# Kernel tuning notes

Measured on AMD Instinct MI355X. Metric: run time of the kernel, lower is better.

The kernel has to match this reference:

```python
import math
import jax, jax.numpy as jnp
import numpy as np

NUM_HEADS = 16
EPS = 1e-6


def _rotate_half(t):
    t1, t2 = jnp.split(t, 2, axis=-1)
    return jnp.concatenate([-t2, t1], axis=-1)


def _rmsnorm(t, w):
    # compute in fp32 like the torch module, then cast back and apply affine
    x32 = t.astype(jnp.float32)
    r = jax.lax.rsqrt(jnp.mean(x32 * x32, axis=-1, keepdims=True) + EPS)
    return (x32 * r).astype(t.dtype) * w


def setup_inputs() -> dict:
    key = jax.random.key(0)
    ks = jax.random.split(key, 12)
    B, N, C, T = 8, 1024, 1024, 1024
    hd2 = (C // NUM_HEADS) // 2  # 32
    inp = {
        "x": jax.random.normal(ks[0], (B, N, C), jnp.float32),
        "temb": jax.random.normal(ks[1], (B, T), jnp.float32),
        "cos_y": jax.random.uniform(ks[2], (1, 1, N, hd2), jnp.float32, -1.0, 1.0),
        "sin_y": jax.random.uniform(ks[3], (1, 1, N, hd2), jnp.float32, -1.0, 1.0),
        "cos_x": jax.random.uniform(ks[4], (1, 1, N, hd2), jnp.float32, -1.0, 1.0),
        "sin_x": jax.random.uniform(ks[5], (1, 1, N, hd2), jnp.float32, -1.0, 1.0),
        # params; weights stored (in, out) so y = x @ W + b (== torch x @ W.T)
        "Wqkv": jax.random.normal(ks[6], (C, 3 * C), jnp.float32) * 0.02,
        "bqkv": jnp.zeros((3 * C,), jnp.float32),
        "Wt": jax.random.normal(ks[7], (T, 3 * C), jnp.float32) * 0.02,
        "bt": jnp.zeros((3 * C,), jnp.float32),
        "Wp": jax.random.normal(ks[8], (C, C), jnp.float32) * 0.02,
        "bp": jnp.zeros((C,), jnp.float32),
        "qn_w": jnp.ones((C // NUM_HEADS,), jnp.float32),
        "kn_w": jnp.ones((C // NUM_HEADS,), jnp.float32),
    }
    return inp


def reference(x, temb, cos_y, sin_y, cos_x, sin_x,
              Wqkv, bqkv, Wt, bt, Wp, bp, qn_w, kn_w):
    B, N, C = x.shape
    H = NUM_HEADS
    hd = C // H
    # fused QKV projection + additive time conditioning
    qkv = x @ Wqkv + bqkv + (temb @ Wt + bt)[:, None, :]         # [B,N,3C]
    qkv = qkv.reshape(B, N, 3, H, hd).transpose(2, 0, 3, 1, 4)    # [3,B,H,N,hd]
    q, k, v = qkv[0], qkv[1], qkv[2]
    # per-head QK RMSNorm with affine
    q = _rmsnorm(q, qn_w)
    k = _rmsnorm(k, kn_w)
    # axial 2D RoPE on the y-half and x-half of head_dim
    qy, qx = jnp.split(q, 2, axis=-1)
    ky, kx = jnp.split(k, 2, axis=-1)
    qy = qy * cos_y + _rotate_half(qy) * sin_y
    ky = ky * cos_y + _rotate_half(ky) * sin_y
    qx = qx * cos_x + _rotate_half(qx) * sin_x
    kx = kx * cos_x + _rotate_half(kx) * sin_x
    q = jnp.concatenate([qy, qx], axis=-1)
    k = jnp.concatenate([ky, kx], axis=-1)
    # scaled dot-product attention (no dropout at eval)
    scale = 1.0 / math.sqrt(hd)
    scores = jnp.einsum('bhqd,bhkd->bhqk', q, k) * scale
    attn = jax.nn.softmax(scores, axis=-1)
    out = jnp.einsum('bhqk,bhkd->bhqd', attn, v)                  # [B,H,N,hd]
    out = out.transpose(0, 2, 1, 3).reshape(B, N, C)
    return out @ Wp + bp
```

## Files before the change

### kernel.cpp

```cpp
#include <hip/hip_runtime.h>
#include <cstdint>

typedef unsigned short u16;
typedef __bf16 bf16x8 __attribute__((ext_vector_type(8)));
typedef float f32x4 __attribute__((ext_vector_type(4)));

__device__ __forceinline__ u16 f2bf(float f) {
  __bf16 h = (__bf16)f;
  return __builtin_bit_cast(u16, h);
}
__device__ __forceinline__ float bf2f(u16 u) {
  union { uint32_t u; float f; } v; v.u = ((uint32_t)u) << 16;
  return v.f;
}

__device__ __forceinline__ void gload16(const void* g, const void* l) {
  __builtin_amdgcn_global_load_lds(
      (const __attribute__((address_space(1))) uint32_t*)(uintptr_t)g,
      (__attribute__((address_space(3))) uint32_t*)(uintptr_t)l, 16, 0, 0);
}

__device__ __forceinline__ f32x4 mfma16(bf16x8 a, bf16x8 b, f32x4 c) {
  return __builtin_amdgcn_mfma_f32_16x16x32_bf16(a, b, c, 0, 0, 0);
}

__device__ __forceinline__ int swz(int row, int col) {
  return row * 64 + ((((col >> 3) ^ (row & 7)) << 3) | (col & 7));
}

__device__ __forceinline__ void transpose64(const float* __restrict__ src,
                                            u16* __restrict__ dst, int R, int Cc,
                                            int r0, int c0, u16* t) {
  #pragma unroll
  for (int i = 0; i < 16; i++) {
    int e = i * 256 + threadIdx.x;
    int rl = e >> 6, cl = e & 63;
    t[cl * 66 + rl] = f2bf(src[(size_t)(r0 + rl) * Cc + c0 + cl]);
  }
  __syncthreads();
  #pragma unroll
  for (int i = 0; i < 16; i++) {
    int e = i * 256 + threadIdx.x;
    int ro = e >> 6, co = e & 63;
    dst[(size_t)(c0 + ro) * R + r0 + co] = t[ro * 66 + co];
  }
}

__global__ __launch_bounds__(256)
void k_prep(const float* __restrict__ x, u16* __restrict__ x_bf,
            const float* __restrict__ Wqkv, u16* __restrict__ WqkvT,
            const float* __restrict__ Wp, u16* __restrict__ WpT,
            const float* __restrict__ temb, const float* __restrict__ Wt,
            float* __restrict__ tpart) {
  __shared__ u16 t[64 * 66];
  int bid = blockIdx.x;
  if (bid < 8192) {
    int i = bid * 256 + threadIdx.x;
    float4 v = ((const float4*)x)[i];
    union { u16 s[4]; uint2 u; } o;
    o.s[0] = f2bf(v.x); o.s[1] = f2bf(v.y); o.s[2] = f2bf(v.z); o.s[3] = f2bf(v.w);
    ((uint2*)x_bf)[i] = o.u;
    return;
  }
  bid -= 8192;
  if (bid < 768) {
    transpose64(Wqkv, WqkvT, 1024, 3072, (bid / 48) * 64, (bid % 48) * 64, t);
    return;
  }
  bid -= 768;
  if (bid < 256) {
    transpose64(Wp, WpT, 1024, 1024, (bid / 16) * 64, (bid % 16) * 64, t);
    return;
  }
  bid -= 256;
  {
    const int j = (bid % 12) * 256 + threadIdx.x;
    const int k0 = (bid / 12) * 32;
    float acc[8];
    #pragma unroll
    for (int b = 0; b < 8; b++) acc[b] = 0.f;
    #pragma unroll 4
    for (int k = k0; k < k0 + 32; k++) {
      float wv = Wt[(size_t)k * 3072 + j];
      #pragma unroll
      for (int b = 0; b < 8; b++) acc[b] += temb[b * 1024 + k] * wv;
    }
    float* p = tpart + (size_t)(bid / 12) * 24576 + j;
    #pragma unroll
    for (int b = 0; b < 8; b++) p[b * 3072] = acc[b];
  }
}

template <int MODE>
__global__ __launch_bounds__(512, 2)
void k_gemm(const u16* __restrict__ A, const u16* __restrict__ Bt,
            u16* __restrict__ outb, float* __restrict__ outf,
            const float* __restrict__ bias,
            const float* __restrict__ bt, const float* __restrict__ bqkv,
            const float* __restrict__ tpart, int K, int Ntot) {
  __shared__ __align__(16) u16 As[3][128 * 64];
  __shared__ __align__(16) u16 Bs[3][256 * 64];
  __shared__ float tcs[256];

  const int nb = (int)gridDim.x;
  const int bid = (int)blockIdx.x;
  const int sb = (bid & 7) * (nb >> 3) + (bid >> 3);
  const int NBN = Ntot >> 8;
  const int m0 = (sb / NBN) * 128;
  const int n0 = (sb % NBN) * 256;

  const int lane = threadIdx.x & 63;
  const int w = threadIdx.x >> 6;
  const int wm = w >> 2;
  const int wn = w & 3;
  const int l15 = lane & 15;
  const int g8 = (lane >> 4) * 8;
  const int lr = lane >> 3;
  const int schunk = ((lane & 7) ^ lr) * 8;

  const u16* Ag = A + (size_t)(m0 + w * 16 + lr) * K + schunk;
  const u16* Bg = Bt + (size_t)(n0 + lr) * K + schunk;

  if (MODE == 0) {
    if (threadIdx.x < 256) {
      const int bidx = m0 >> 10;
      const int j = n0 + (int)threadIdx.x;
      float a = bt[j] + bqkv[j];
      #pragma unroll
      for (int kt = 0; kt < 32; kt++) a += tpart[(size_t)kt * 24576 + bidx * 3072 + j];
      tcs[threadIdx.x] = a;
    }
    asm volatile("" ::: "memory");
  }

  f32x4 acc[4][4];
  #pragma unroll
  for (int i = 0; i < 4; i++)
    #pragma unroll
    for (int j = 0; j < 4; j++) acc[i][j] = (f32x4){0.f, 0.f, 0.f, 0.f};

  auto stageA_Blo = [&](int kt_, int buf_) {
    const int ko = kt_ << 6;
    #pragma unroll
    for (int t = 0; t < 2; t++) {
      int r0 = w * 16 + t * 8;
      gload16(Ag + (size_t)(t * 8) * K + ko, &As[buf_][r0 * 64]);
    }
    #pragma unroll
    for (int t = 0; t < 2; t++) {
      int f0 = w * 16 + t * 8;
      int r0 = (f0 >> 5) * 64 + (f0 & 31);
      gload16(Bg + (size_t)r0 * K + ko, &Bs[buf_][r0 * 64]);
    }
  };
  auto stageBhi = [&](int kt_, int buf_) {
    const int ko = kt_ << 6;
    #pragma unroll
    for (int t = 0; t < 2; t++) {
      int f0 = w * 16 + t * 8;
      int r0 = (f0 >> 5) * 64 + 32 + (f0 & 31);
      gload16(Bg + (size_t)r0 * K + ko, &Bs[buf_][r0 * 64]);
    }
  };

  const int NT = K >> 6;
  stageA_Blo(0, 0); stageBhi(0, 0);
  stageA_Blo(1, 1); stageBhi(1, 1);
  asm volatile("s_waitcnt vmcnt(8)" ::: "memory");
  __builtin_amdgcn_s_barrier();
  asm volatile("" ::: "memory");

  int cur = 0;
  for (int kt = 0; kt < NT; kt++) {
    const int nxtbuf = cur + 2 >= 3 ? cur - 1 : cur + 2;

    bf16x8 af[2][4], bfr[2][4];
    #pragma unroll
    for (int s = 0; s < 2; s++)
      #pragma unroll
      for (int mf = 0; mf < 4; mf++)
        af[s][mf] = *(const bf16x8*)&As[cur][swz(wm * 64 + mf * 16 + l15, s * 32 + g8)];
    #pragma unroll
    for (int s = 0; s < 2; s++)
      #pragma unroll
      for (int nf = 0; nf < 2; nf++)
        bfr[s][nf] = *(const bf16x8*)&Bs[cur][swz(wn * 64 + nf * 16 + l15, s * 32 + g8)];
    if (kt + 2 < NT) stageA_Blo(kt + 2, nxtbuf);
    if (kt <= NT - 2) asm volatile("s_waitcnt vmcnt(6)" ::: "memory");
    else              asm volatile("s_waitcnt vmcnt(0)" ::: "memory");
    __builtin_amdgcn_s_barrier();
    asm volatile("" ::: "memory");
    __builtin_amdgcn_s_setprio(1);
    #pragma unroll
    for (int s = 0; s < 2; s++)
      #pragma unroll
      for (int mf = 0; mf < 4; mf++)
        #pragma unroll
        for (int nf = 0; nf < 2; nf++)
          acc[mf][nf] = mfma16(af[s][mf], bfr[s][nf], acc[mf][nf]);
    __builtin_amdgcn_s_setprio(0);

    #pragma unroll
    for (int s = 0; s < 2; s++)
      #pragma unroll
      for (int nf = 2; nf < 4; nf++)
        bfr[s][nf] = *(const bf16x8*)&Bs[cur][swz(wn * 64 + nf * 16 + l15, s * 32 + g8)];
    if (kt + 2 < NT) stageBhi(kt + 2, nxtbuf);
    if (kt < NT - 2)       asm volatile("s_waitcnt vmcnt(6)" ::: "memory");
    else if (kt == NT - 2) asm volatile("s_waitcnt vmcnt(2)" ::: "memory");
    else                   asm volatile("s_waitcnt vmcnt(0)" ::: "memory");
    __builtin_amdgcn_s_barrier();
    asm volatile("" ::: "memory");
    __builtin_amdgcn_s_setprio(1);
    #pragma unroll
    for (int s = 0; s < 2; s++)
      #pragma unroll
      for (int mf = 0; mf < 4; mf++)
        #pragma unroll
        for (int nf = 2; nf < 4; nf++)
          acc[mf][nf] = mfma16(af[s][mf], bfr[s][nf], acc[mf][nf]);
    __builtin_amdgcn_s_setprio(0);

    cur = cur + 1 >= 3 ? 0 : cur + 1;
  }

  const int rl = (lane >> 4) * 4;
  #pragma unroll
  for (int mf = 0; mf < 4; mf++) {
    #pragma unroll
    for (int nf = 0; nf < 4; nf++) {
      #pragma unroll
      for (int r = 0; r < 4; r++) {
        int grow = m0 + wm * 64 + mf * 16 + rl + r;
        int gcol = n0 + wn * 64 + nf * 16 + l15;
        float v = acc[mf][nf][r];
        if (MODE == 0) {
          v += tcs[wn * 64 + nf * 16 + l15];
          outb[(size_t)grow * Ntot + gcol] = f2bf(v);
        } else {
          v += bias[gcol];
          outf[(size_t)grow * Ntot + gcol] = v;
        }
      }
    }
  }
}

__global__ __launch_bounds__(256)
void k_rrv(const u16* __restrict__ qkv,
           const float* __restrict__ cos_y, const float* __restrict__ sin_y,
           const float* __restrict__ cos_x, const float* __restrict__ sin_x,
           const float* __restrict__ qn_w, const float* __restrict__ kn_w,
           u16* __restrict__ Qo, u16* __restrict__ Ko, u16* __restrict__ VT) {
  __shared__ u16 t[64 * 68];
  const int n0 = blockIdx.x * 64, h = blockIdx.y, b = blockIdx.z;
  const int bh = b * 16 + h;
  const int lane = threadIdx.x & 63, w = threadIdx.x >> 6;
  const int l15 = lane & 15, lg = lane >> 4;
  float4 qw = *(const float4*)(qn_w + l15 * 4);
  float4 kw = *(const float4*)(kn_w + l15 * 4);
  const float sgn = (lane & 4) ? 1.0f : -1.0f;
  const float* ct = (lane & 8) ? cos_x : cos_y;
  const float* st = (lane & 8) ? sin_x : sin_y;
  const float QSCALE = 0.18033688011112042f;

  #pragma unroll
  for (int rr = 0; rr < 4; rr++) {
    int row = n0 + w * 16 + rr * 4 + lg;
    size_t src = (size_t)(b * 1024 + row) * 3072 + h * 64 + l15 * 4;
    uint2 qu = *(const uint2*)(qkv + src);
    uint2 ku = *(const uint2*)(qkv + src + 1024);
    float q[4], k[4];
    q[0] = bf2f((u16)qu.x); q[1] = bf2f((u16)(qu.x >> 16));
    q[2] = bf2f((u16)qu.y); q[3] = bf2f((u16)(qu.y >> 16));
    k[0] = bf2f((u16)ku.x); k[1] = bf2f((u16)(ku.x >> 16));
    k[2] = bf2f((u16)ku.y); k[3] = bf2f((u16)(ku.y >> 16));
    float sq = q[0]*q[0] + q[1]*q[1] + q[2]*q[2] + q[3]*q[3];
    float sk = k[0]*k[0] + k[1]*k[1] + k[2]*k[2] + k[3]*k[3];
    #pragma unroll
    for (int m = 1; m < 16; m <<= 1) {
      sq += __shfl_xor(sq, m);
      sk += __shfl_xor(sk, m);
    }
    float rq = rsqrtf(sq * (1.0f / 64.0f) + 1e-6f);
    float rk = rsqrtf(sk * (1.0f / 64.0f) + 1e-6f);
    float4 cc = *(const float4*)(ct + (size_t)row * 32 + (lane & 7) * 4);
    float4 ss = *(const float4*)(st + (size_t)row * 32 + (lane & 7) * 4);
    float qn[4], kn[4];
    qn[0] = q[0]*rq*qw.x; qn[1] = q[1]*rq*qw.y; qn[2] = q[2]*rq*qw.z; qn[3] = q[3]*rq*qw.w;
    kn[0] = k[0]*rk*kw.x; kn[1] = k[1]*rk*kw.y; kn[2] = k[2]*rk*kw.z; kn[3] = k[3]*rk*kw.w;
    float c[4] = {cc.x, cc.y, cc.z, cc.w};
    float s[4] = {ss.x, ss.y, ss.z, ss.w};
    union { u16 e[4]; uint2 u; } oq, ok;
    #pragma unroll
    for (int j = 0; j < 4; j++) {
      float qp = __shfl_xor(qn[j], 4);
      float kp = __shfl_xor(kn[j], 4);
      oq.e[j] = f2bf((qn[j] * c[j] + sgn * qp * s[j]) * QSCALE);
      ok.e[j] = f2bf(kn[j] * c[j] + sgn * kp * s[j]);
    }
    size_t dst = ((size_t)bh * 1024 + row) * 64 + l15 * 4;
    *(uint2*)(Qo + dst) = oq.u;
    *(uint2*)(Ko + dst) = ok.u;
  }

  #pragma unroll
  for (int i = 0; i < 4; i++) {
    int e = i * 256 + threadIdx.x;
    int n = e >> 4, dc = e & 15;
    uint2 v = *(const uint2*)(qkv + (size_t)(b * 1024 + n0 + n) * 3072 + 2048 + h * 64 + dc * 4);
    t[(dc * 4 + 0) * 68 + n] = (u16)v.x;
    t[(dc * 4 + 1) * 68 + n] = (u16)(v.x >> 16);
    t[(dc * 4 + 2) * 68 + n] = (u16)v.y;
    t[(dc * 4 + 3) * 68 + n] = (u16)(v.y >> 16);
  }
  __syncthreads();
  #pragma unroll
  for (int i = 0; i < 4; i++) {
    int e = i * 256 + threadIdx.x;
    int d = e >> 4, nc = e & 15;
    const u16* p = &t[d * 68 + nc * 4];
    uint2 o;
    o.x = (uint32_t)p[0] | ((uint32_t)p[1] << 16);
    o.y = (uint32_t)p[2] | ((uint32_t)p[3] << 16);
    *(uint2*)(VT + ((size_t)bh * 64 + d) * 1024 + n0 + nc * 4) = o;
  }
}

__global__ __launch_bounds__(256, 2)
void k_attn(const u16* __restrict__ Q, const u16* __restrict__ Kb,
            const u16* __restrict__ VT, u16* __restrict__ Ob) {
  __shared__ u16 Ks[2][4096], VTs[2][4096], Ps[4][2048];
  const int lane = threadIdx.x & 63;
  const int w = threadIdx.x >> 6;
  const int bh = blockIdx.x;
  const int qt = blockIdx.y;
  const int b = bh >> 4, h = bh & 15;
  const size_t base = (size_t)bh * 65536;
  const int q0 = qt * 128;
  const int scol = ((lane & 7) ^ (lane >> 3)) * 8;
  const int lr = lane >> 3;

  bf16x8 aq[2][2];
  #pragma unroll
  for (int i = 0; i < 2; i++)
    #pragma unroll
    for (int s = 0; s < 2; s++)
      aq[i][s] = *(const bf16x8*)(Q + base +
          (size_t)(q0 + w * 32 + i * 16 + (lane & 15)) * 64 + s * 32 + (lane >> 4) * 8);

  f32x4 acc_o[2][4];
  float lpar[2][4];
  #pragma unroll
  for (int i = 0; i < 2; i++)
    #pragma unroll
    for (int r = 0; r < 4; r++) {
      acc_o[i][r] = (f32x4){0.f, 0.f, 0.f, 0.f};
      lpar[i][r] = 0.f;
    }

  #pragma unroll
  for (int tt = 0; tt < 2; tt++) {
    int t = w * 2 + tt;
    gload16(Kb + base + (size_t)(8 * t + lr) * 64 + scol, &Ks[0][t * 512]);
    gload16(VT + base + (size_t)(8 * t + lr) * 1024 + scol, &VTs[0][t * 512]);
  }

  for (int it = 0; it < 16; it++) {
    __syncthreads();
    const int cur = it & 1;
    if (it < 15) {
      const int nxt = cur ^ 1;
      const int j1 = (it + 1) * 64;
      #pragma unroll
      for (int tt = 0; tt < 2; tt++) {
        int t = w * 2 + tt;
        gload16(Kb + base + (size_t)(j1 + 8 * t + lr) * 64 + scol, &Ks[nxt][t * 512]);
        gload16(VT + base + (size_t)(8 * t + lr) * 1024 + j1 + scol, &VTs[nxt][t * 512]);
      }
    }
    const u16* K_ = Ks[cur];
    const u16* V_ = VTs[cur];

    f32x4 accs[2][4];
    #pragma unroll
    for (int i = 0; i < 2; i++)
      #pragma unroll
      for (int nt = 0; nt < 4; nt++) accs[i][nt] = (f32x4){0.f, 0.f, 0.f, 0.f};
    #pragma unroll
    for (int s = 0; s < 2; s++) {
      bf16x8 bk[4];
      #pragma unroll
      for (int nt = 0; nt < 4; nt++)
        bk[nt] = *(const bf16x8*)&K_[swz(nt * 16 + (lane & 15), s * 32 + (lane >> 4) * 8)];
      __builtin_amdgcn_s_setprio(1);
      #pragma unroll
      for (int i = 0; i < 2; i++)
        #pragma unroll
        for (int nt = 0; nt < 4; nt++)
          accs[i][nt] = mfma16(aq[i][s], bk[nt], accs[i][nt]);
      __builtin_amdgcn_s_setprio(0);
    }

    #pragma unroll
    for (int i = 0; i < 2; i++) {
      #pragma unroll
      for (int nt = 0; nt < 4; nt++) {
        #pragma unroll
        for (int r = 0; r < 4; r++) {
          float p = __builtin_amdgcn_exp2f(accs[i][nt][r]);
          lpar[i][r] += p;
          Ps[w][swz(i * 16 + (lane >> 4) * 4 + r, nt * 16 + (lane & 15))] = f2bf(p);
        }
      }
    }
    asm volatile("s_waitcnt lgkmcnt(0)" ::: "memory");

    #pragma unroll
    for (int s = 0; s < 2; s++) {
      bf16x8 bv[4];
      #pragma unroll
      for (int dt = 0; dt < 4; dt++)
        bv[dt] = *(const bf16x8*)&V_[swz(dt * 16 + (lane & 15), s * 32 + (lane >> 4) * 8)];
      bf16x8 ap0 = *(const bf16x8*)&Ps[w][swz(0 * 16 + (lane & 15), s * 32 + (lane >> 4) * 8)];
      bf16x8 ap1 = *(const bf16x8*)&Ps[w][swz(1 * 16 + (lane & 15), s * 32 + (lane >> 4) * 8)];
      __builtin_amdgcn_s_setprio(1);
      #pragma unroll
      for (int dt = 0; dt < 4; dt++) {
        acc_o[0][dt] = mfma16(ap0, bv[dt], acc_o[0][dt]);
        acc_o[1][dt] = mfma16(ap1, bv[dt], acc_o[1][dt]);
      }
      __builtin_amdgcn_s_setprio(0);
    }
  }

  #pragma unroll
  for (int i = 0; i < 2; i++) {
    float inv[4];
    #pragma unroll
    for (int r = 0; r < 4; r++) {
      float l = lpar[i][r];
      #pragma unroll
      for (int m = 1; m < 16; m <<= 1) l += __shfl_xor(l, m);
      inv[r] = 1.0f / l;
    }
    #pragma unroll
    for (int dt = 0; dt < 4; dt++)
      #pragma unroll
      for (int r = 0; r < 4; r++) {
        int row = q0 + w * 32 + i * 16 + (lane >> 4) * 4 + r;
        int col = h * 64 + dt * 16 + (lane & 15);
        Ob[((size_t)b * 1024 + row) * 1024 + col] = f2bf(acc_o[i][dt][r] * inv[r]);
      }
  }
}

extern "C" void kernel_launch(void* const* d_in, const int* in_sizes, int n_in,
                              void* d_out, int out_size, void* d_ws, size_t ws_size,
                              hipStream_t stream) {
  const float* x     = (const float*)d_in[0];
  const float* temb  = (const float*)d_in[1];
  const float* cos_y = (const float*)d_in[2];
  const float* sin_y = (const float*)d_in[3];
  const float* cos_x = (const float*)d_in[4];
  const float* sin_x = (const float*)d_in[5];
  const float* Wqkv  = (const float*)d_in[6];
  const float* bqkv  = (const float*)d_in[7];
  const float* Wt    = (const float*)d_in[8];
  const float* bt    = (const float*)d_in[9];
  const float* Wp    = (const float*)d_in[10];
  const float* bp    = (const float*)d_in[11];
  const float* qn_w  = (const float*)d_in[12];
  const float* kn_w  = (const float*)d_in[13];
  float* out = (float*)d_out;

  char* ws = (char*)d_ws;
  u16*   x_bf  = (u16*)(ws);
  u16*   WqkvT = (u16*)(ws + 16777216);
  u16*   WpT   = (u16*)(ws + 23068672);
  u16*   qkv   = (u16*)(ws + 25264128);
  u16*   Qb    = (u16*)(ws + 75595776);
  u16*   Kb    = (u16*)(ws + 92372992);
  u16*   VTb   = (u16*)(ws + 109150208);
  float* tpart = (float*)(ws + 125927424);
  u16*   att   = x_bf;

  k_prep<<<9600, 256, 0, stream>>>(x, x_bf, Wqkv, WqkvT, Wp, WpT, temb, Wt, tpart);
  k_gemm<0><<<dim3(768), 512, 0, stream>>>(x_bf, WqkvT, qkv, nullptr, nullptr,
                                           bt, bqkv, tpart, 1024, 3072);
  k_rrv<<<dim3(16, 16, 8), 256, 0, stream>>>(qkv, cos_y, sin_y, cos_x, sin_x,
                                             qn_w, kn_w, Qb, Kb, VTb);
  k_attn<<<dim3(128, 8), 256, 0, stream>>>(Qb, Kb, VTb, att);
  k_gemm<1><<<dim3(256), 512, 0, stream>>>(att, WpT, nullptr, out, bp,
                                           nullptr, nullptr, nullptr, 1024, 1024);
}
```

Measured before the change: 273.2 us.

## Replace QKV GEMM with 256x128-tile kernel and keep attention P in registers

The QKV projection gets a new dedicated GEMM kernel: 256x128 tiles, 256 threads, K-step 32, double-buffered LDS. The old triple-buffered 128x256 template remains only for the output projection. In attention, S is computed transposed (K as the A operand), so the exponentiated probabilities are packed straight into bf16 MFMA A-fragments with v_cvt_pk_bf16_f32. This removes the per-wave LDS round trip for P and its wait. V fragments are now read as two 8-byte pieces, and the row-sum reduction changes to match the transposed layout. The risks are the new GEMM's different pipelining depth and tile shape, and the correctness of the new fragment layout.

```diff
diff --git a/kernel.cpp b/kernel.cpp
--- a/kernel.cpp
+++ b/kernel.cpp
@@ -91,16 +91,107 @@
   }
 }
 
-template <int MODE>
+__global__ __launch_bounds__(256, 2)
+void k_gemm0(const u16* __restrict__ A, const u16* __restrict__ Bt,
+             u16* __restrict__ outb,
+             const float* __restrict__ bt, const float* __restrict__ bqkv,
+             const float* __restrict__ tpart, int K, int Ntot) {
+  __shared__ u16 As[2][8192];
+  __shared__ u16 Bs[2][4096];
+  __shared__ float tcs[128];
+  const int m0 = blockIdx.y * 256;
+  const int n0 = blockIdx.x * 128;
+  const int lane = threadIdx.x & 63;
+  const int w = threadIdx.x >> 6;
+  const int l15 = lane & 15;
+  const int fo = (((lane >> 4) ^ ((lane >> 1) & 3)) << 3);
+  const int srow = lane >> 2;
+  const int schunk = (((lane & 3) ^ ((lane >> 3) & 3)) << 3);
+
+  if (threadIdx.x < 128) {
+    const int bidx = m0 >> 10;
+    const int j = n0 + (int)threadIdx.x;
+    float a = bt[j] + bqkv[j];
+    #pragma unroll
+    for (int kt = 0; kt < 32; kt++) a += tpart[(size_t)kt * 24576 + bidx * 3072 + j];
+    tcs[threadIdx.x] = a;
+  }
+  asm volatile("" ::: "memory");
+
+  f32x4 acc[4][8];
+  #pragma unroll
+  for (int i = 0; i < 4; i++)
+    #pragma unroll
+    for (int j = 0; j < 8; j++) acc[i][j] = (f32x4){0.f, 0.f, 0.f, 0.f};
+
+  const u16* Ag = A + (size_t)(m0 + srow) * K + schunk;
+  const u16* Bg = Bt + (size_t)(n0 + srow) * K + schunk;
+
+  const int iters = K >> 5;
+  #pragma unroll
+  for (int tt = 0; tt < 4; tt++) {
+    int t = w * 4 + tt;
+    gload16(Ag + (size_t)(16 * t) * K, &As[0][t * 512]);
+  }
+  #pragma unroll
+  for (int tt = 0; tt < 2; tt++) {
+    int t = w * 2 + tt;
+    gload16(Bg + (size_t)(16 * t) * K, &Bs[0][t * 512]);
+  }
+
+  for (int it = 0; it < iters; it++) {
+    __syncthreads();
+    const int cur = it & 1;
+    if (it + 1 < iters) {
+      const int nxt = cur ^ 1;
+      const int k1 = (it + 1) << 5;
+      #pragma unroll
+      for (int tt = 0; tt < 4; tt++) {
+        int t = w * 4 + tt;
+        gload16(Ag + (size_t)(16 * t) * K + k1, &As[nxt][t * 512]);
+      }
+      #pragma unroll
+      for (int tt = 0; tt < 2; tt++) {
+        int t = w * 2 + tt;
+        gload16(Bg + (size_t)(16 * t) * K + k1, &Bs[nxt][t * 512]);
+      }
+    }
+    bf16x8 af[4], bfr[8];
+    #pragma unroll
+    for (int i = 0; i < 4; i++)
+      af[i] = *(const bf16x8*)&As[cur][(w * 64 + 16 * i + l15) * 32 + fo];
+    #pragma unroll
+    for (int j = 0; j < 8; j++)
+      bfr[j] = *(const bf16x8*)&Bs[cur][(16 * j + l15) * 32 + fo];
+    #pragma unroll
+    for (int i = 0; i < 4; i++)
+      #pragma unroll
+      for (int j = 0; j < 8; j++)
+        acc[i][j] = mfma16(af[i], bfr[j], acc[i][j]);
+  }
+
+  const int rl = (lane >> 4) * 4;
+  #pragma unroll
+  for (int i = 0; i < 4; i++) {
+    #pragma unroll
+    for (int j = 0; j < 8; j++) {
+      #pragma unroll
+      for (int r = 0; r < 4; r++) {
+        int grow = m0 + w * 64 + 16 * i + rl + r;
+        int gcol = n0 + 16 * j + l15;
+        float v = acc[i][j][r] + tcs[16 * j + l15];
+        outb[(size_t)grow * Ntot + gcol] = f2bf(v);
+      }
+    }
+  }
+}
+
 __global__ __launch_bounds__(512, 2)
-void k_gemm(const u16* __restrict__ A, const u16* __restrict__ Bt,
-            u16* __restrict__ outb, float* __restrict__ outf,
-            const float* __restrict__ bias,
-            const float* __restrict__ bt, const float* __restrict__ bqkv,
-            const float* __restrict__ tpart, int K, int Ntot) {
+void k_gemm1(const u16* __restrict__ A, const u16* __restrict__ Bt,
+             float* __restrict__ outf, const float* __restrict__ bias,
+             int K, int Ntot) {
   __shared__ __align__(16) u16 As[3][128 * 64];
   __shared__ __align__(16) u16 Bs[3][256 * 64];
-  __shared__ float tcs[256];
 
   const int nb = (int)gridDim.x;
   const int bid = (int)blockIdx.x;
@@ -120,18 +211,6 @@
 
   const u16* Ag = A + (size_t)(m0 + w * 16 + lr) * K + schunk;
   const u16* Bg = Bt + (size_t)(n0 + lr) * K + schunk;
-
-  if (MODE == 0) {
-    if (threadIdx.x < 256) {
-      const int bidx = m0 >> 10;
-      const int j = n0 + (int)threadIdx.x;
-      float a = bt[j] + bqkv[j];
-      #pragma unroll
-      for (int kt = 0; kt < 32; kt++) a += tpart[(size_t)kt * 24576 + bidx * 3072 + j];
-      tcs[threadIdx.x] = a;
-    }
-    asm volatile("" ::: "memory");
-  }
 
   f32x4 acc[4][4];
   #pragma unroll
@@ -233,14 +312,7 @@
       for (int r = 0; r < 4; r++) {
         int grow = m0 + wm * 64 + mf * 16 + rl + r;
         int gcol = n0 + wn * 64 + nf * 16 + l15;
-        float v = acc[mf][nf][r];
-        if (MODE == 0) {
-          v += tcs[wn * 64 + nf * 16 + l15];
-          outb[(size_t)grow * Ntot + gcol] = f2bf(v);
-        } else {
-          v += bias[gcol];
-          outf[(size_t)grow * Ntot + gcol] = v;
-        }
+        outf[(size_t)grow * Ntot + gcol] = acc[mf][nf][r] + bias[gcol];
       }
     }
   }
@@ -330,7 +402,7 @@
 __global__ __launch_bounds__(256, 2)
 void k_attn(const u16* __restrict__ Q, const u16* __restrict__ Kb,
             const u16* __restrict__ VT, u16* __restrict__ Ob) {
-  __shared__ u16 Ks[2][4096], VTs[2][4096], Ps[4][2048];
+  __shared__ u16 Ks[2][4096], VTs[2][4096];
   const int lane = threadIdx.x & 63;
   const int w = threadIdx.x >> 6;
   const int bh = blockIdx.x;
@@ -340,6 +412,8 @@
   const int q0 = qt * 128;
   const int scol = ((lane & 7) ^ (lane >> 3)) * 8;
   const int lr = lane >> 3;
+  const int l15 = lane & 15;
+  const int g = lane >> 4;
 
   bf16x8 aq[2][2];
   #pragma unroll
@@ -347,17 +421,14 @@
     #pragma unroll
     for (int s = 0; s < 2; s++)
       aq[i][s] = *(const bf16x8*)(Q + base +
-          (size_t)(q0 + w * 32 + i * 16 + (lane & 15)) * 64 + s * 32 + (lane >> 4) * 8);
+          (size_t)(q0 + w * 32 + i * 16 + l15) * 64 + s * 32 + g * 8);
 
   f32x4 acc_o[2][4];
-  float lpar[2][4];
+  float lpar[2] = {0.f, 0.f};
   #pragma unroll
   for (int i = 0; i < 2; i++)
     #pragma unroll
-    for (int r = 0; r < 4; r++) {
-      acc_o[i][r] = (f32x4){0.f, 0.f, 0.f, 0.f};
-      lpar[i][r] = 0.f;
-    }
+    for (int dt = 0; dt < 4; dt++) acc_o[i][dt] = (f32x4){0.f, 0.f, 0.f, 0.f};
 
   #pragma unroll
   for (int tt = 0; tt < 2; tt++) {
@@ -392,43 +463,51 @@
       bf16x8 bk[4];
       #pragma unroll
       for (int nt = 0; nt < 4; nt++)
-        bk[nt] = *(const bf16x8*)&K_[swz(nt * 16 + (lane & 15), s * 32 + (lane >> 4) * 8)];
+        bk[nt] = *(const bf16x8*)&K_[swz(nt * 16 + l15, s * 32 + g * 8)];
       __builtin_amdgcn_s_setprio(1);
       #pragma unroll
       for (int i = 0; i < 2; i++)
         #pragma unroll
         for (int nt = 0; nt < 4; nt++)
-          accs[i][nt] = mfma16(aq[i][s], bk[nt], accs[i][nt]);
+          accs[i][nt] = mfma16(bk[nt], aq[i][s], accs[i][nt]);
       __builtin_amdgcn_s_setprio(0);
     }
 
-    #pragma unroll
-    for (int i = 0; i < 2; i++) {
-      #pragma unroll
-      for (int nt = 0; nt < 4; nt++) {
+    float p[2][4][4];
+    #pragma unroll
+    for (int i = 0; i < 2; i++)
+      #pragma unroll
+      for (int nt = 0; nt < 4; nt++)
         #pragma unroll
         for (int r = 0; r < 4; r++) {
-          float p = __builtin_amdgcn_exp2f(accs[i][nt][r]);
-          lpar[i][r] += p;
-          Ps[w][swz(i * 16 + (lane >> 4) * 4 + r, nt * 16 + (lane & 15))] = f2bf(p);
+          p[i][nt][r] = __builtin_amdgcn_exp2f(accs[i][nt][r]);
+          lpar[i] += p[i][nt][r];
         }
-      }
-    }
-    asm volatile("s_waitcnt lgkmcnt(0)" ::: "memory");
 
     #pragma unroll
     for (int s = 0; s < 2; s++) {
+      union { uint32_t u[4]; bf16x8 v; } ap[2];
+      #pragma unroll
+      for (int i = 0; i < 2; i++)
+        #pragma unroll
+        for (int m = 0; m < 4; m++)
+          asm("v_cvt_pk_bf16_f32 %0, %1, %2"
+              : "=v"(ap[i].u[m])
+              : "v"(p[i][2 * s + (m >> 1)][2 * (m & 1)]),
+                "v"(p[i][2 * s + (m >> 1)][2 * (m & 1) + 1]));
       bf16x8 bv[4];
       #pragma unroll
-      for (int dt = 0; dt < 4; dt++)
-        bv[dt] = *(const bf16x8*)&V_[swz(dt * 16 + (lane & 15), s * 32 + (lane >> 4) * 8)];
-      bf16x8 ap0 = *(const bf16x8*)&Ps[w][swz(0 * 16 + (lane & 15), s * 32 + (lane >> 4) * 8)];
-      bf16x8 ap1 = *(const bf16x8*)&Ps[w][swz(1 * 16 + (lane & 15), s * 32 + (lane >> 4) * 8)];
+      for (int dt = 0; dt < 4; dt++) {
+        union { uint2 x2[2]; bf16x8 v; } bb;
+        bb.x2[0] = *(const uint2*)&V_[swz(dt * 16 + l15, s * 32 + 4 * g)];
+        bb.x2[1] = *(const uint2*)&V_[swz(dt * 16 + l15, s * 32 + 16 + 4 * g)];
+        bv[dt] = bb.v;
+      }
       __builtin_amdgcn_s_setprio(1);
       #pragma unroll
       for (int dt = 0; dt < 4; dt++) {
-        acc_o[0][dt] = mfma16(ap0, bv[dt], acc_o[0][dt]);
-        acc_o[1][dt] = mfma16(ap1, bv[dt], acc_o[1][dt]);
+        acc_o[0][dt] = mfma16(ap[0].v, bv[dt], acc_o[0][dt]);
+        acc_o[1][dt] = mfma16(ap[1].v, bv[dt], acc_o[1][dt]);
       }
       __builtin_amdgcn_s_setprio(0);
     }
@@ -436,20 +515,21 @@
 
   #pragma unroll
   for (int i = 0; i < 2; i++) {
+    float lred = lpar[i];
+    lred += __shfl_xor(lred, 16);
+    lred += __shfl_xor(lred, 32);
     float inv[4];
     #pragma unroll
     for (int r = 0; r < 4; r++) {
-      float l = lpar[i][r];
-      #pragma unroll
-      for (int m = 1; m < 16; m <<= 1) l += __shfl_xor(l, m);
-      inv[r] = 1.0f / l;
+      float lv = __shfl(lred, 4 * g + r);
+      inv[r] = 1.0f / lv;
     }
     #pragma unroll
     for (int dt = 0; dt < 4; dt++)
       #pragma unroll
       for (int r = 0; r < 4; r++) {
-        int row = q0 + w * 32 + i * 16 + (lane >> 4) * 4 + r;
-        int col = h * 64 + dt * 16 + (lane & 15);
+        int row = q0 + w * 32 + i * 16 + 4 * g + r;
+        int col = h * 64 + dt * 16 + l15;
         Ob[((size_t)b * 1024 + row) * 1024 + col] = f2bf(acc_o[i][dt][r] * inv[r]);
       }
   }
@@ -486,11 +566,10 @@
   u16*   att   = x_bf;
 
   k_prep<<<9600, 256, 0, stream>>>(x, x_bf, Wqkv, WqkvT, Wp, WpT, temb, Wt, tpart);
-  k_gemm<0><<<dim3(768), 512, 0, stream>>>(x_bf, WqkvT, qkv, nullptr, nullptr,
-                                           bt, bqkv, tpart, 1024, 3072);
+  k_gemm0<<<dim3(24, 32), 256, 0, stream>>>(x_bf, WqkvT, qkv, bt, bqkv, tpart,
+                                            1024, 3072);
   k_rrv<<<dim3(16, 16, 8), 256, 0, stream>>>(qkv, cos_y, sin_y, cos_x, sin_x,
                                              qn_w, kn_w, Qb, Kb, VTb);
   k_attn<<<dim3(128, 8), 256, 0, stream>>>(Qb, Kb, VTb, att);
-  k_gemm<1><<<dim3(256), 512, 0, stream>>>(att, WpT, nullptr, out, bp,
-                                           nullptr, nullptr, nullptr, 1024, 1024);
-}
+  k_gemm1<<<dim3(256), 512, 0, stream>>>(att, WpT, out, bp, 1024, 1024);
+}
```

Result: no change. 269.5 us (-1.3%).
